# Optimization experiments

Hardware: AMD Instinct MI355X
Metric: run time of the kernel (lower is better)

The kernel has to match this reference:

```python
import jax, jax.numpy as jnp
import numpy as np
import math

ANCHOR_RATIO = 0.1
MIN_ANCHORS = 1


def setup_inputs() -> dict:
    key = jax.random.key(0)
    k1, k2 = jax.random.split(key)
    patches = jax.random.normal(k1, (16, 1024, 256, 64), dtype=jnp.float32)  # [b, n, p, d]
    adp = jax.random.uniform(k2, (1024, 1024), dtype=jnp.float32)            # [n, n]
    return {"patches": patches, "adp": adp}


def reference(patches, adp):
    b, n, p, d = patches.shape
    # anchor_count = min(max(min_anchors, ceil(p * anchor_ratio)), p) -- static
    k = min(max(MIN_ANCHORS, int(math.ceil(p * ANCHOR_RATIO))), p)
    importance = adp.mean(axis=0)                                  # [n]
    norms = jnp.sqrt(jnp.sum(patches * patches, axis=-1))          # [b, n, p]
    scores = jnp.einsum('bnp,n->bp', norms, importance)            # [b, p]
    _, topk_idx = jax.lax.top_k(scores, k)                         # [b, k]
    mean_tokens = patches.mean(axis=1)                             # [b, p, d]
    anchors = jnp.take_along_axis(mean_tokens, topk_idx[:, :, None], axis=1)  # [b, k, d]
    # repeat per node then concat over batch -> [b*n, k, d]
    anchors = jnp.broadcast_to(anchors[:, None], (b, n, k, d)).reshape(b * n, k, d)
    return anchors
```

## Files before the change

kernel.cpp:

```cpp
#include <hip/hip_runtime.h>

#define B_SZ   16
#define N_NODES 1024
#define P_TOK  256
#define D_DIM  64
#define K_ANCH 26

__global__ void k_importance(const float* __restrict__ adp,
                             float* __restrict__ imp) {
    int j = blockIdx.x * blockDim.x + threadIdx.x;
    float s = 0.f;
    #pragma unroll 8
    for (int i = 0; i < N_NODES; ++i)
        s += adp[i * N_NODES + j];
    imp[j] = s * (1.0f / N_NODES);
}

__global__ __launch_bounds__(64)
void k_scores_means(const float* __restrict__ patches,
                    const float* __restrict__ imp,
                    float* __restrict__ scores,
                    float4* __restrict__ mean4) {
    __shared__ float s_imp[N_NODES];
    int t = threadIdx.x;
    for (int i = t; i < N_NODES; i += 64) s_imp[i] = imp[i];
    __syncthreads();

    int b  = blockIdx.x >> 8;
    int p  = blockIdx.x & 255;
    int g  = t >> 4;
    int d4 = t & 15;

    const float4* base = (const float4*)patches;
    unsigned row0 = ((unsigned)b * N_NODES) * P_TOK + (unsigned)p;

    float4 macc = make_float4(0.f, 0.f, 0.f, 0.f);
    float score = 0.f;

    #pragma unroll 4
    for (int n0 = 0; n0 < N_NODES; n0 += 4) {
        int n = n0 + g;
        float4 v = base[(size_t)(row0 + (unsigned)n * P_TOK) * 16u + (unsigned)d4];
        macc.x += v.x; macc.y += v.y; macc.z += v.z; macc.w += v.w;
        float sq = v.x * v.x + v.y * v.y + v.z * v.z + v.w * v.w;
        sq += __shfl_xor(sq, 1);
        sq += __shfl_xor(sq, 2);
        sq += __shfl_xor(sq, 4);
        sq += __shfl_xor(sq, 8);
        score += sqrtf(sq) * s_imp[n];
    }

    score += __shfl_xor(score, 16);
    score += __shfl_xor(score, 32);
    macc.x += __shfl_xor(macc.x, 16);  macc.x += __shfl_xor(macc.x, 32);
    macc.y += __shfl_xor(macc.y, 16);  macc.y += __shfl_xor(macc.y, 32);
    macc.z += __shfl_xor(macc.z, 16);  macc.z += __shfl_xor(macc.z, 32);
    macc.w += __shfl_xor(macc.w, 16);  macc.w += __shfl_xor(macc.w, 32);

    if (t < 16) {
        const float inv = 1.0f / N_NODES;
        float4 m = make_float4(macc.x * inv, macc.y * inv, macc.z * inv, macc.w * inv);
        mean4[(size_t)(b * P_TOK + p) * 16 + d4] = m;
    }
    if (t == 0)
        scores[b * P_TOK + p] = score;
}

__global__ __launch_bounds__(P_TOK)
void k_topk(const float* __restrict__ scores, int* __restrict__ topk) {
    __shared__ float s[P_TOK];
    int b = blockIdx.x;
    int j = threadIdx.x;
    float v = scores[b * P_TOK + j];
    s[j] = v;
    __syncthreads();
    int rank = 0;
    #pragma unroll 8
    for (int i = 0; i < P_TOK; ++i) {
        float si = s[i];
        rank += (si > v) || (si == v && i < j);
    }
    if (rank < K_ANCH)
        topk[b * K_ANCH + rank] = j;
}

__global__ __launch_bounds__(64)
void k_gather(const float* __restrict__ mean_t,
              const int* __restrict__ topk,
              float* __restrict__ anchors) {
    int pair = blockIdx.x;
    int b = pair / K_ANCH;
    int idx = topk[pair];
    anchors[pair * D_DIM + threadIdx.x] =
        mean_t[((size_t)(b * P_TOK + idx)) * D_DIM + threadIdx.x];
}

__global__ void k_broadcast(const float4* __restrict__ anchors4,
                            float4* __restrict__ out4,
                            unsigned total4) {
    const unsigned PER_B = (unsigned)N_NODES * K_ANCH * D_DIM / 4;
    const unsigned ROW4  = (unsigned)K_ANCH * D_DIM / 4;
    unsigned stride = gridDim.x * blockDim.x;
    for (unsigned f = blockIdx.x * blockDim.x + threadIdx.x; f < total4; f += stride) {
        unsigned b = f / PER_B;
        unsigned r = f % ROW4;
        out4[f] = anchors4[b * ROW4 + r];
    }
}

extern "C" void kernel_launch(void* const* d_in, const int* in_sizes, int n_in,
                              void* d_out, int out_size, void* d_ws, size_t ws_size,
                              hipStream_t stream) {
    const float* patches = (const float*)d_in[0];
    const float* adp     = (const float*)d_in[1];
    float* out = (float*)d_out;

    char* ws = (char*)d_ws;
    float* imp     = (float*)(ws + 0);
    float* scores  = (float*)(ws + 4096);
    int*   topk    = (int*)  (ws + 4096 + 16384);
    float* anchors = (float*)(ws + 4096 + 16384 + 2048);

    float* mean_t = out;

    k_importance<<<dim3(N_NODES / 256), dim3(256), 0, stream>>>(adp, imp);

    k_scores_means<<<dim3(B_SZ * P_TOK), dim3(64), 0, stream>>>(
        patches, imp, scores, (float4*)mean_t);

    k_topk<<<dim3(B_SZ), dim3(P_TOK), 0, stream>>>(scores, topk);

    k_gather<<<dim3(B_SZ * K_ANCH), dim3(64), 0, stream>>>(mean_t, topk, anchors);

    unsigned total4 = (unsigned)out_size / 4;
    k_broadcast<<<dim3(4096), dim3(256), 0, stream>>>(
        (const float4*)anchors, (float4*)out, total4);
}
```

Measured before the change: 1.450 ms.

## Split importance reduction, widen score blocks, fuse top-k with gather

The adp column-mean becomes a two-stage reduction over 16 row chunks, so 64 blocks do the work instead of 4. The scores/means kernel uses 256 threads per (b,p), with four waves each covering a quarter of the nodes and combining through shared memory, which raises memory parallelism per block. Top-k and gather are merged into one kernel, removing a launch and the topk index buffer. The cost is one extra launch for the final importance reduction and an added shared-memory sync.

```diff
diff --git a/kernel.cpp b/kernel.cpp
--- a/kernel.cpp
+++ b/kernel.cpp
@@ -1,46 +1,64 @@
 #include <hip/hip_runtime.h>
 
-#define B_SZ   16
+#define B_SZ    16
 #define N_NODES 1024
-#define P_TOK  256
-#define D_DIM  64
-#define K_ANCH 26
+#define P_TOK   256
+#define D_DIM   64
+#define K_ANCH  26
 
-__global__ void k_importance(const float* __restrict__ adp,
-                             float* __restrict__ imp) {
-    int j = blockIdx.x * blockDim.x + threadIdx.x;
+__global__ __launch_bounds__(256)
+void k_imp_partial(const float* __restrict__ adp, float* __restrict__ partial) {
+    int j  = blockIdx.x * 256 + threadIdx.x;
+    int rc = blockIdx.y;
+    const float* src = adp + (size_t)rc * 64 * N_NODES + j;
     float s = 0.f;
     #pragma unroll 8
-    for (int i = 0; i < N_NODES; ++i)
-        s += adp[i * N_NODES + j];
+    for (int i = 0; i < 64; ++i)
+        s += src[i * N_NODES];
+    partial[rc * N_NODES + j] = s;
+}
+
+__global__ __launch_bounds__(256)
+void k_imp_final(const float* __restrict__ partial, float* __restrict__ imp) {
+    int j = blockIdx.x * 256 + threadIdx.x;
+    float s = 0.f;
+    #pragma unroll
+    for (int rc = 0; rc < 16; ++rc)
+        s += partial[rc * N_NODES + j];
     imp[j] = s * (1.0f / N_NODES);
 }
 
-__global__ __launch_bounds__(64)
+__global__ __launch_bounds__(256)
 void k_scores_means(const float* __restrict__ patches,
                     const float* __restrict__ imp,
                     float* __restrict__ scores,
                     float4* __restrict__ mean4) {
-    __shared__ float s_imp[N_NODES];
+    __shared__ float  s_imp[N_NODES];
+    __shared__ float4 s_macc[4][16];
+    __shared__ float  s_score[4];
+
     int t = threadIdx.x;
-    for (int i = t; i < N_NODES; i += 64) s_imp[i] = imp[i];
+    for (int i = t; i < N_NODES; i += 256) s_imp[i] = imp[i];
     __syncthreads();
 
-    int b  = blockIdx.x >> 8;
-    int p  = blockIdx.x & 255;
-    int g  = t >> 4;
-    int d4 = t & 15;
+    int b    = blockIdx.x >> 8;
+    int p    = blockIdx.x & 255;
+    int w    = t >> 6;
+    int lane = t & 63;
+    int g    = lane >> 4;
+    int d4   = lane & 15;
 
-    const float4* base = (const float4*)patches;
-    unsigned row0 = ((unsigned)b * N_NODES) * P_TOK + (unsigned)p;
+    const float4* base = (const float4*)patches
+                       + ((size_t)b * N_NODES * P_TOK + p) * 16 + d4;
 
     float4 macc = make_float4(0.f, 0.f, 0.f, 0.f);
     float score = 0.f;
+    int nbase = w * 256;
 
-    #pragma unroll 4
-    for (int n0 = 0; n0 < N_NODES; n0 += 4) {
-        int n = n0 + g;
-        float4 v = base[(size_t)(row0 + (unsigned)n * P_TOK) * 16u + (unsigned)d4];
+    #pragma unroll 8
+    for (int n0 = 0; n0 < 256; n0 += 4) {
+        int n = nbase + n0 + g;
+        float4 v = base[(size_t)n * (P_TOK * 16)];
         macc.x += v.x; macc.y += v.y; macc.z += v.z; macc.w += v.w;
         float sq = v.x * v.x + v.y * v.y + v.z * v.z + v.w * v.w;
         sq += __shfl_xor(sq, 1);
@@ -57,17 +75,27 @@
     macc.z += __shfl_xor(macc.z, 16);  macc.z += __shfl_xor(macc.z, 32);
     macc.w += __shfl_xor(macc.w, 16);  macc.w += __shfl_xor(macc.w, 32);
 
+    if (lane < 16) s_macc[w][d4] = macc;
+    if (lane == 0) s_score[w] = score;
+    __syncthreads();
+
     if (t < 16) {
+        float4 a = s_macc[0][t], b2 = s_macc[1][t], c = s_macc[2][t], d = s_macc[3][t];
         const float inv = 1.0f / N_NODES;
-        float4 m = make_float4(macc.x * inv, macc.y * inv, macc.z * inv, macc.w * inv);
-        mean4[(size_t)(b * P_TOK + p) * 16 + d4] = m;
+        float4 m = make_float4((a.x + b2.x + c.x + d.x) * inv,
+                               (a.y + b2.y + c.y + d.y) * inv,
+                               (a.z + b2.z + c.z + d.z) * inv,
+                               (a.w + b2.w + c.w + d.w) * inv);
+        mean4[(size_t)(b * P_TOK + p) * 16 + t] = m;
     }
     if (t == 0)
-        scores[b * P_TOK + p] = score;
+        scores[b * P_TOK + p] = s_score[0] + s_score[1] + s_score[2] + s_score[3];
 }
 
 __global__ __launch_bounds__(P_TOK)
-void k_topk(const float* __restrict__ scores, int* __restrict__ topk) {
+void k_topk_gather(const float* __restrict__ scores,
+                   const float4* __restrict__ mean4,
+                   float4* __restrict__ anchors4) {
     __shared__ float s[P_TOK];
     int b = blockIdx.x;
     int j = threadIdx.x;
@@ -80,24 +108,18 @@
         float si = s[i];
         rank += (si > v) || (si == v && i < j);
     }
-    if (rank < K_ANCH)
-        topk[b * K_ANCH + rank] = j;
+    if (rank < K_ANCH) {
+        const float4* src = mean4   + (size_t)(b * P_TOK + j)     * 16;
+        float4*       dst = anchors4 + (size_t)(b * K_ANCH + rank) * 16;
+        #pragma unroll
+        for (int i = 0; i < 16; ++i) dst[i] = src[i];
+    }
 }
 
-__global__ __launch_bounds__(64)
-void k_gather(const float* __restrict__ mean_t,
-              const int* __restrict__ topk,
-              float* __restrict__ anchors) {
-    int pair = blockIdx.x;
-    int b = pair / K_ANCH;
-    int idx = topk[pair];
-    anchors[pair * D_DIM + threadIdx.x] =
-        mean_t[((size_t)(b * P_TOK + idx)) * D_DIM + threadIdx.x];
-}
-
-__global__ void k_broadcast(const float4* __restrict__ anchors4,
-                            float4* __restrict__ out4,
-                            unsigned total4) {
+__global__ __launch_bounds__(256)
+void k_broadcast(const float4* __restrict__ anchors4,
+                 float4* __restrict__ out4,
+                 unsigned total4) {
     const unsigned PER_B = (unsigned)N_NODES * K_ANCH * D_DIM / 4;
     const unsigned ROW4  = (unsigned)K_ANCH * D_DIM / 4;
     unsigned stride = gridDim.x * blockDim.x;
@@ -118,19 +140,19 @@
     char* ws = (char*)d_ws;
     float* imp     = (float*)(ws + 0);
     float* scores  = (float*)(ws + 4096);
-    int*   topk    = (int*)  (ws + 4096 + 16384);
-    float* anchors = (float*)(ws + 4096 + 16384 + 2048);
+    float* partial = (float*)(ws + 20480);
+    float* anchors = (float*)(ws + 86016);
 
-    float* mean_t = out;
+    float4* mean4 = (float4*)out;
 
-    k_importance<<<dim3(N_NODES / 256), dim3(256), 0, stream>>>(adp, imp);
+    k_imp_partial<<<dim3(N_NODES / 256, 16), dim3(256), 0, stream>>>(adp, partial);
+    k_imp_final  <<<dim3(N_NODES / 256),     dim3(256), 0, stream>>>(partial, imp);
 
-    k_scores_means<<<dim3(B_SZ * P_TOK), dim3(64), 0, stream>>>(
-        patches, imp, scores, (float4*)mean_t);
+    k_scores_means<<<dim3(B_SZ * P_TOK), dim3(256), 0, stream>>>(
+        patches, imp, scores, mean4);
 
-    k_topk<<<dim3(B_SZ), dim3(P_TOK), 0, stream>>>(scores, topk);
-
-    k_gather<<<dim3(B_SZ * K_ANCH), dim3(64), 0, stream>>>(mean_t, topk, anchors);
+    k_topk_gather<<<dim3(B_SZ), dim3(P_TOK), 0, stream>>>(
+        scores, mean4, (float4*)anchors);
 
     unsigned total4 = (unsigned)out_size / 4;
     k_broadcast<<<dim3(4096), dim3(256), 0, stream>>>(
```

Result: faster. 1.380 ms (-4.8%).
